# Optimization experiments

Measured on AMD Instinct MI355X. Metric: run time of the kernel, lower is better.

Reference implementation:

```python
import jax, jax.numpy as jnp
import numpy as np

N_NODES = 40000
N_EDGES = 400000
N_GRAPHS = 128
IN_F = 768
HID = 128
HEADS = 4
NEG_SLOPE = 0.2  # DGL GATConv default


def _p(key, shape, scale=0.02):
    return jax.random.normal(key, shape, dtype=jnp.float32) * scale


def setup_inputs() -> dict:
    key = jax.random.key(0)
    ks = jax.random.split(key, 20)
    x = jax.random.normal(ks[0], (N_NODES, IN_F), dtype=jnp.float32)
    src = jax.random.randint(ks[1], (N_EDGES,), 0, N_NODES)
    dst = jax.random.randint(ks[2], (N_EDGES,), 0, N_NODES)
    graph_ids = jnp.sort(jax.random.randint(ks[3], (N_NODES,), 0, N_GRAPHS))
    params = {
        # GAT layer 1: 768 -> 4 heads x 128
        "W1": _p(ks[4], (IN_F, HEADS * HID)),
        "al1": _p(ks[5], (HEADS, HID)),
        "ar1": _p(ks[6], (HEADS, HID)),
        "b1": jnp.zeros((HEADS * HID,), jnp.float32),
        # GAT layer 2: 512 -> 1 head x 128
        "W2": _p(ks[7], (HEADS * HID, HID)),
        "al2": _p(ks[8], (1, HID)),
        "ar2": _p(ks[9], (1, HID)),
        "b2": jnp.zeros((HID,), jnp.float32),
        # node MLP: 128 -> 128 -> 2
        "nW1": _p(ks[10], (HID, HID)), "nb1": jnp.zeros((HID,), jnp.float32),
        "nW2": _p(ks[11], (HID, 2)), "nb2": jnp.zeros((2,), jnp.float32),
        # graph MLP: 128 -> 128 -> 2
        "gW1": _p(ks[12], (HID, HID)), "gb1": jnp.zeros((HID,), jnp.float32),
        "gW2": _p(ks[13], (HID, 2)), "gb2": jnp.zeros((2,), jnp.float32),
    }
    return dict(x=x, src=src, dst=dst, graph_ids=graph_ids, **params)


def gat_conv(h, W, attn_l, attn_r, bias, src, dst, heads, out_f):
    # DGL GATConv (eval mode, no dropout): project, per-edge attention logits,
    # segment softmax over incoming edges of each dst node, weighted scatter-add.
    feat = (h @ W).reshape(N_NODES, heads, out_f)           # [N,H,F]
    el = jnp.einsum('nhf,hf->nh', feat, attn_l)              # [N,H]
    er = jnp.einsum('nhf,hf->nh', feat, attn_r)              # [N,H]
    e = el[src] + er[dst]                                    # [E,H]
    e = jnp.where(e > 0, e, NEG_SLOPE * e)                   # LeakyReLU(0.2)
    emax = jax.ops.segment_max(e, dst, num_segments=N_NODES)  # [N,H], -inf for empty
    ee = jnp.exp(e - emax[dst])                              # [E,H]
    denom = jax.ops.segment_sum(ee, dst, num_segments=N_NODES)  # [N,H]
    alpha = ee / denom[dst]                                  # [E,H]
    msg = feat[src] * alpha[:, :, None]                      # [E,H,F]
    out = jax.ops.segment_sum(msg, dst, num_segments=N_NODES)  # [N,H,F]
    return out + bias.reshape(1, heads, out_f)


def reference(x, src, dst, graph_ids, W1, al1, ar1, b1, W2, al2, ar2, b2,
              nW1, nb1, nW2, nb2, gW1, gb1, gW2, gb2):
    h = gat_conv(x, W1, al1, ar1, b1, src, dst, HEADS, HID)   # [N,4,128]
    h = h.reshape(N_NODES, HEADS * HID)                       # flatten(1)
    h = gat_conv(h, W2, al2, ar2, b2, src, dst, 1, HID)       # [N,1,128]
    h = h.squeeze(1)                                          # [N,128]
    # dgl.mean_nodes over batched graphs
    cnt = jax.ops.segment_sum(jnp.ones((N_NODES,), h.dtype), graph_ids, num_segments=N_GRAPHS)
    hg = jax.ops.segment_sum(h, graph_ids, num_segments=N_GRAPHS) / jnp.maximum(cnt, 1.0)[:, None]
    node_logits = jax.nn.relu(h @ nW1 + nb1) @ nW2 + nb2      # [N,2]
    graph_logits = jax.nn.relu(hg @ gW1 + gb1) @ gW2 + gb2    # [G,2]
    return node_logits, graph_logits
```

## Files before the change

kernel.cpp:

```cpp
#include <hip/hip_runtime.h>
#include <cstddef>

#define NN 40000
#define NE 400000
#define NG 128
#define NB_SCAN 157

typedef __attribute__((ext_vector_type(8))) short bf16x8;
typedef __attribute__((ext_vector_type(4))) float f32x4;

__device__ __forceinline__ void split1(float x, unsigned short& h, unsigned short& l)
{
    unsigned u = __float_as_uint(x);
    unsigned rh = u + 0x7FFFu + ((u >> 16) & 1u);
    h = (unsigned short)(rh >> 16);
    float fh = __uint_as_float(((unsigned)h) << 16);
    float r = x - fh;
    unsigned u2 = __float_as_uint(r);
    unsigned rl = u2 + 0x7FFFu + ((u2 >> 16) & 1u);
    l = (unsigned short)(rl >> 16);
}

__global__ void conv_bt(const float* __restrict__ B, unsigned short* __restrict__ hi,
                        unsigned short* __restrict__ lo, int K, int N)
{
    int e = blockIdx.x * 256 + threadIdx.x;
    if (e >= K * N) return;
    int n = e / K, k = e - n * K;
    unsigned short h, l;
    split1(B[(size_t)k * N + n], h, l);
    hi[e] = h; lo[e] = l;
}

#define LDK 40

__global__ __launch_bounds__(256) void gemm_split(
    const float* __restrict__ A, const unsigned short* __restrict__ Bh,
    const unsigned short* __restrict__ Bl, float* __restrict__ C,
    int M, int K, int N)
{
    __shared__ unsigned short Ah_s[128 * LDK];
    __shared__ unsigned short Al_s[128 * LDK];
    __shared__ unsigned short Bh_s[128 * LDK];
    __shared__ unsigned short Bl_s[128 * LDK];

    const int t    = threadIdx.x;
    const int lane = t & 63;
    const int wid  = t >> 6;
    const int wr   = wid >> 1, wc = wid & 1;
    const int bm   = blockIdx.x * 128, bn = blockIdx.y * 128;

    const int sr = t >> 1;
    const int sk = (t & 1) * 16;

    const int arow = bm + sr;
    const bool aval = (arow < M);
    const float* Ap = A + (size_t)arow * K + sk;
    const unsigned short* Bhp = Bh + (size_t)(bn + sr) * K + sk;
    const unsigned short* Blp = Bl + (size_t)(bn + sr) * K + sk;

    f32x4 acc[4][4];
    #pragma unroll
    for (int i = 0; i < 4; ++i)
        #pragma unroll
        for (int j = 0; j < 4; ++j) acc[i][j] = (f32x4){0.f, 0.f, 0.f, 0.f};

    float4 abuf[4];
    uint4 bhbuf[2], blbuf[2];
    const int NT = K / 32;

    auto load_tile = [&](int kt) {
        const int kb = kt * 32;
        if (aval) {
            #pragma unroll
            for (int q = 0; q < 4; ++q) abuf[q] = *(const float4*)(Ap + kb + q * 4);
        } else {
            #pragma unroll
            for (int q = 0; q < 4; ++q) abuf[q] = make_float4(0.f, 0.f, 0.f, 0.f);
        }
        bhbuf[0] = *(const uint4*)(Bhp + kb);
        bhbuf[1] = *(const uint4*)(Bhp + kb + 8);
        blbuf[0] = *(const uint4*)(Blp + kb);
        blbuf[1] = *(const uint4*)(Blp + kb + 8);
    };

    auto store_tile = [&]() {
        unsigned short h[16], l[16];
        #pragma unroll
        for (int q = 0; q < 4; ++q) {
            split1(abuf[q].x, h[q * 4 + 0], l[q * 4 + 0]);
            split1(abuf[q].y, h[q * 4 + 1], l[q * 4 + 1]);
            split1(abuf[q].z, h[q * 4 + 2], l[q * 4 + 2]);
            split1(abuf[q].w, h[q * 4 + 3], l[q * 4 + 3]);
        }
        *(uint4*)&Ah_s[sr * LDK + sk]     = *(uint4*)&h[0];
        *(uint4*)&Ah_s[sr * LDK + sk + 8] = *(uint4*)&h[8];
        *(uint4*)&Al_s[sr * LDK + sk]     = *(uint4*)&l[0];
        *(uint4*)&Al_s[sr * LDK + sk + 8] = *(uint4*)&l[8];
        *(uint4*)&Bh_s[sr * LDK + sk]     = bhbuf[0];
        *(uint4*)&Bh_s[sr * LDK + sk + 8] = bhbuf[1];
        *(uint4*)&Bl_s[sr * LDK + sk]     = blbuf[0];
        *(uint4*)&Bl_s[sr * LDK + sk + 8] = blbuf[1];
    };

    auto compute = [&]() {
        const int fr = lane & 15;
        const int fk = (lane >> 4) * 8;
        bf16x8 bhf[4], blf[4];
        #pragma unroll
        for (int ni = 0; ni < 4; ++ni) {
            bhf[ni] = *(bf16x8*)&Bh_s[(wc * 64 + ni * 16 + fr) * LDK + fk];
            blf[ni] = *(bf16x8*)&Bl_s[(wc * 64 + ni * 16 + fr) * LDK + fk];
        }
        #pragma unroll
        for (int mi = 0; mi < 4; ++mi) {
            bf16x8 ah = *(bf16x8*)&Ah_s[(wr * 64 + mi * 16 + fr) * LDK + fk];
            bf16x8 al = *(bf16x8*)&Al_s[(wr * 64 + mi * 16 + fr) * LDK + fk];
            #pragma unroll
            for (int ni = 0; ni < 4; ++ni) {
                acc[mi][ni] = __builtin_amdgcn_mfma_f32_16x16x32_bf16(ah, bhf[ni], acc[mi][ni], 0, 0, 0);
                acc[mi][ni] = __builtin_amdgcn_mfma_f32_16x16x32_bf16(ah, blf[ni], acc[mi][ni], 0, 0, 0);
                acc[mi][ni] = __builtin_amdgcn_mfma_f32_16x16x32_bf16(al, bhf[ni], acc[mi][ni], 0, 0, 0);
            }
        }
    };

    load_tile(0);
    store_tile();
    __syncthreads();
    for (int kt = 0;;) {
        if (kt + 1 < NT) load_tile(kt + 1);
        compute();
        ++kt;
        if (kt == NT) break;
        __syncthreads();
        store_tile();
        __syncthreads();
    }

    const int fr = lane & 15;
    const int fq = lane >> 4;
    #pragma unroll
    for (int mi = 0; mi < 4; ++mi) {
        int r0 = bm + wr * 64 + mi * 16 + fq * 4;
        #pragma unroll
        for (int ni = 0; ni < 4; ++ni) {
            int c = bn + wc * 64 + ni * 16 + fr;
            #pragma unroll
            for (int q = 0; q < 4; ++q) {
                int r = r0 + q;
                if (r < M) C[(size_t)r * N + c] = acc[mi][ni][q];
            }
        }
    }
}

__global__ void hist_kernel(const int* __restrict__ dst, int* __restrict__ cnt)
{
    int e = blockIdx.x * 256 + threadIdx.x;
    if (e < NE) atomicAdd(&cnt[dst[e]], 1);
}

__global__ __launch_bounds__(256) void scanA_kernel(
    const int* __restrict__ cnt, int* __restrict__ row, int* __restrict__ bsum)
{
    __shared__ int s[256];
    int t = threadIdx.x;
    int i = blockIdx.x * 256 + t;
    int v = (i < NN) ? cnt[i] : 0;
    s[t] = v;
    __syncthreads();
    #pragma unroll
    for (int off = 1; off < 256; off <<= 1) {
        int x = (t >= off) ? s[t - off] : 0;
        __syncthreads();
        s[t] += x;
        __syncthreads();
    }
    if (i < NN) row[i] = s[t] - v;
    if (t == 255) bsum[blockIdx.x] = s[255];
}

__global__ __launch_bounds__(256) void scanB_kernel(int* __restrict__ bsum)
{
    __shared__ int s[256];
    int t = threadIdx.x;
    int v = (t < NB_SCAN) ? bsum[t] : 0;
    s[t] = v;
    __syncthreads();
    #pragma unroll
    for (int off = 1; off < 256; off <<= 1) {
        int x = (t >= off) ? s[t - off] : 0;
        __syncthreads();
        s[t] += x;
        __syncthreads();
    }
    if (t < NB_SCAN) bsum[t] = s[t] - v;
}

__global__ void scanC_kernel(int* __restrict__ row, const int* __restrict__ bsum,
                             int* __restrict__ fill)
{
    int i = blockIdx.x * 256 + threadIdx.x;
    if (i < NN) {
        int r = row[i] + bsum[blockIdx.x];
        row[i] = r;
        fill[i] = r;
    }
    if (i == 0) row[NN] = NE;
}

__global__ void permute_kernel(const int* __restrict__ dst, int* __restrict__ fill,
                               int* __restrict__ eidx)
{
    int e = blockIdx.x * 256 + threadIdx.x;
    if (e < NE) {
        int pos = atomicAdd(&fill[dst[e]], 1);
        eidx[pos] = e;
    }
}

template <int H>
__global__ __launch_bounds__(256) void eler_kernel(
    const float* __restrict__ feat, const float* __restrict__ al,
    const float* __restrict__ ar, float* __restrict__ el, float* __restrict__ er)
{
    int wid  = (blockIdx.x * 256 + threadIdx.x) >> 6;
    int lane = threadIdx.x & 63;
    if (wid >= NN * H) return;
    int n = wid / H, h = wid % H;
    const float* f = feat + (size_t)n * (H * 128) + h * 128;
    float2 fv = *(const float2*)&f[lane * 2];
    float2 a1 = *(const float2*)&al[h * 128 + lane * 2];
    float2 a2 = *(const float2*)&ar[h * 128 + lane * 2];
    float sl = fv.x * a1.x + fv.y * a1.y;
    float sr = fv.x * a2.x + fv.y * a2.y;
    #pragma unroll
    for (int off = 32; off > 0; off >>= 1) {
        sl += __shfl_down(sl, off);
        sr += __shfl_down(sr, off);
    }
    if (lane == 0) { el[wid] = sl; er[wid] = sr; }
}

template <int H>
__global__ __launch_bounds__(256) void edge_w_kernel(
    const int* __restrict__ src, const int* __restrict__ dst,
    const float* __restrict__ el, const float* __restrict__ er,
    float* __restrict__ w)
{
    int e = blockIdx.x * 256 + threadIdx.x;
    if (e >= NE) return;
    int s = src[e], d = dst[e];
    if constexpr (H == 4) {
        float4 a = *(const float4*)&el[s * 4];
        float4 b = *(const float4*)&er[d * 4];
        float4 v = make_float4(a.x + b.x, a.y + b.y, a.z + b.z, a.w + b.w);
        v.x = v.x > 0.f ? v.x : 0.2f * v.x;
        v.y = v.y > 0.f ? v.y : 0.2f * v.y;
        v.z = v.z > 0.f ? v.z : 0.2f * v.z;
        v.w = v.w > 0.f ? v.w : 0.2f * v.w;
        *(float4*)&w[e * 4] = make_float4(__expf(v.x), __expf(v.y), __expf(v.z), __expf(v.w));
    } else {
        float v = el[s] + er[d];
        v = v > 0.f ? v : 0.2f * v;
        w[e] = __expf(v);
    }
}

template <int H>
__global__ __launch_bounds__(256) void agg_kernel(
    const int* __restrict__ row, const int* __restrict__ eidx,
    const int* __restrict__ src, const float* __restrict__ w,
    const float* __restrict__ feat, const float* __restrict__ bias,
    float* __restrict__ out)
{
    int wave = (blockIdx.x * 256 + threadIdx.x) >> 6;
    int lane = threadIdx.x & 63;
    if (wave >= NN) return;
    int r0 = row[wave], r1 = row[wave + 1];

    if constexpr (H == 4) {
        float d0 = 0.f, d1 = 0.f, d2 = 0.f, d3 = 0.f;
        for (int i = r0 + lane; i < r1; i += 64) {
            float4 wv = *(const float4*)&w[eidx[i] * 4];
            d0 += wv.x; d1 += wv.y; d2 += wv.z; d3 += wv.w;
        }
        #pragma unroll
        for (int off = 32; off > 0; off >>= 1) {
            d0 += __shfl_xor(d0, off);
            d1 += __shfl_xor(d1, off);
            d2 += __shfl_xor(d2, off);
            d3 += __shfl_xor(d3, off);
        }
        float4 a0 = {0.f,0.f,0.f,0.f}, a1 = {0.f,0.f,0.f,0.f};
        for (int i = r0; i < r1; ++i) {
            int e = eidx[i];
            int s = src[e];
            float4 wv = *(const float4*)&w[e * 4];
            const float* f = feat + (size_t)s * 512;
            float4 v0 = *(const float4*)&f[lane * 4];
            float4 v1 = *(const float4*)&f[256 + lane * 4];
            float alo = (lane & 32) ? wv.y : wv.x;
            float ahi = (lane & 32) ? wv.w : wv.z;
            a0.x = fmaf(v0.x, alo, a0.x); a0.y = fmaf(v0.y, alo, a0.y);
            a0.z = fmaf(v0.z, alo, a0.z); a0.w = fmaf(v0.w, alo, a0.w);
            a1.x = fmaf(v1.x, ahi, a1.x); a1.y = fmaf(v1.y, ahi, a1.y);
            a1.z = fmaf(v1.z, ahi, a1.z); a1.w = fmaf(v1.w, ahi, a1.w);
        }
        float ilo = (lane & 32) ? d1 : d0;
        float ihi = (lane & 32) ? d3 : d2;
        ilo = (r1 > r0) ? 1.0f / ilo : 0.0f;
        ihi = (r1 > r0) ? 1.0f / ihi : 0.0f;
        float4 b0 = *(const float4*)&bias[lane * 4];
        float4 b1v = *(const float4*)&bias[256 + lane * 4];
        float* o = out + (size_t)wave * 512;
        *(float4*)&o[lane * 4] = make_float4(
            fmaf(a0.x, ilo, b0.x), fmaf(a0.y, ilo, b0.y),
            fmaf(a0.z, ilo, b0.z), fmaf(a0.w, ilo, b0.w));
        *(float4*)&o[256 + lane * 4] = make_float4(
            fmaf(a1.x, ihi, b1v.x), fmaf(a1.y, ihi, b1v.y),
            fmaf(a1.z, ihi, b1v.z), fmaf(a1.w, ihi, b1v.w));
    } else {
        float den = 0.f;
        for (int i = r0 + lane; i < r1; i += 64) den += w[eidx[i]];
        #pragma unroll
        for (int off = 32; off > 0; off >>= 1) den += __shfl_xor(den, off);
        float2 a = {0.f, 0.f};
        for (int i = r0; i < r1; ++i) {
            int e = eidx[i];
            int s = src[e];
            float wv = w[e];
            float2 v = *(const float2*)&feat[(size_t)s * 128 + lane * 2];
            a.x = fmaf(v.x, wv, a.x);
            a.y = fmaf(v.y, wv, a.y);
        }
        float inv = (r1 > r0) ? 1.0f / den : 0.0f;
        float2 b = *(const float2*)&bias[lane * 2];
        float* o = out + (size_t)wave * 128;
        *(float2*)&o[lane * 2] = make_float2(fmaf(a.x, inv, b.x), fmaf(a.y, inv, b.y));
    }
}

__global__ __launch_bounds__(128) void graph_mean_kernel(
    const int* __restrict__ gid, const float* __restrict__ h2, float* __restrict__ hg)
{
    int g = blockIdx.x;
    int t = threadIdx.x;
    int lo = 0, hi = NN;
    while (lo < hi) { int m = (lo + hi) >> 1; if (gid[m] < g) lo = m + 1; else hi = m; }
    int start = lo;
    lo = start; hi = NN;
    while (lo < hi) { int m = (lo + hi) >> 1; if (gid[m] < g + 1) lo = m + 1; else hi = m; }
    int end = lo;
    float acc = 0.f;
    for (int n = start; n < end; ++n) acc += h2[(size_t)n * 128 + t];
    float c = fmaxf((float)(end - start), 1.0f);
    hg[g * 128 + t] = acc / c;
}

__global__ __launch_bounds__(128) void node_mlp_kernel(
    const float* __restrict__ h, const float* __restrict__ W1,
    const float* __restrict__ b1, const float* __restrict__ W2,
    const float* __restrict__ b2, float* __restrict__ out)
{
    __shared__ float row[128];
    __shared__ float hid[128];
    int n = blockIdx.x;
    int t = threadIdx.x;
    row[t] = h[(size_t)n * 128 + t];
    __syncthreads();
    float acc = b1[t];
    #pragma unroll 8
    for (int k = 0; k < 128; ++k) acc = fmaf(row[k], W1[k * 128 + t], acc);
    hid[t] = fmaxf(acc, 0.f);
    __syncthreads();
    if (t < 2) {
        float o = b2[t];
        for (int k = 0; k < 128; ++k) o = fmaf(hid[k], W2[k * 2 + t], o);
        out[(size_t)n * 2 + t] = o;
    }
}

__global__ __launch_bounds__(128) void graph_mlp_kernel(
    const float* __restrict__ hg,
    const float* __restrict__ W1, const float* __restrict__ b1,
    const float* __restrict__ W2, const float* __restrict__ b2,
    float* __restrict__ out)
{
    __shared__ float row[128];
    __shared__ float hid[128];
    int g = blockIdx.x;
    int t = threadIdx.x;
    row[t] = hg[(size_t)g * 128 + t];
    __syncthreads();
    float acc = b1[t];
    #pragma unroll 8
    for (int k = 0; k < 128; ++k) acc = fmaf(row[k], W1[k * 128 + t], acc);
    hid[t] = fmaxf(acc, 0.f);
    __syncthreads();
    if (t < 2) {
        float o = b2[t];
        for (int k = 0; k < 128; ++k) o = fmaf(hid[k], W2[k * 2 + t], o);
        out[(size_t)g * 2 + t] = o;
    }
}

static constexpr size_t O_FEAT1 = 0;
static constexpr size_t O_H1    = 20480000;
static constexpr size_t O_H2    = 5120000;
static constexpr size_t O_B2T   = 10240000;
static constexpr size_t O_EW    = 40960000;
static constexpr size_t O_HG    = 42880000;
static constexpr size_t O_INT   = 42896384;
static constexpr size_t I_ROW  = 0;
static constexpr size_t I_BSUM = 40064;
static constexpr size_t I_CNT  = 40224;
static constexpr size_t I_FILL = 80224;
static constexpr size_t I_EIDX = 120224;

extern "C" void kernel_launch(void* const* d_in, const int* in_sizes, int n_in,
                              void* d_out, int out_size, void* d_ws, size_t ws_size,
                              hipStream_t stream)
{
    const float* x    = (const float*)d_in[0];
    const int*   src  = (const int*)d_in[1];
    const int*   dst  = (const int*)d_in[2];
    const int*   gid  = (const int*)d_in[3];
    const float* W1   = (const float*)d_in[4];
    const float* al1  = (const float*)d_in[5];
    const float* ar1  = (const float*)d_in[6];
    const float* b1   = (const float*)d_in[7];
    const float* W2   = (const float*)d_in[8];
    const float* al2  = (const float*)d_in[9];
    const float* ar2  = (const float*)d_in[10];
    const float* b2   = (const float*)d_in[11];
    const float* nW1  = (const float*)d_in[12];
    const float* nb1  = (const float*)d_in[13];
    const float* nW2  = (const float*)d_in[14];
    const float* nb2  = (const float*)d_in[15];
    const float* gW1  = (const float*)d_in[16];
    const float* gb1  = (const float*)d_in[17];
    const float* gW2  = (const float*)d_in[18];
    const float* gb2  = (const float*)d_in[19];
    float* out = (float*)d_out;
    float* ws  = (float*)d_ws;

    float* feat1 = ws + O_FEAT1;
    float* h1    = ws + O_H1;
    float* feat2 = ws + O_FEAT1;
    float* h2    = ws + O_H2;
    float* el1   = ws + O_EW;
    float* er1   = ws + O_EW + 160000;
    float* w1e   = ws + O_EW + 320000;
    float* el2   = ws + O_EW;
    float* er2   = ws + O_EW + 40000;
    float* w2e   = ws + O_EW + 80000;
    float* hg    = ws + O_HG;
    int*   ibase = (int*)(ws + O_INT);
    int*   row   = ibase + I_ROW;
    int*   bsum  = ibase + I_BSUM;
    int*   cnt   = ibase + I_CNT;
    int*   fill  = ibase + I_FILL;
    int*   eidx  = ibase + I_EIDX;

    unsigned short* B1h = (unsigned short*)(ws + O_H1);
    unsigned short* B1l = B1h + 512 * 768;
    unsigned short* B2h = (unsigned short*)(ws + O_B2T);
    unsigned short* B2l = B2h + 128 * 512;

    hipMemsetAsync(cnt, 0, NN * sizeof(int), stream);
    hist_kernel<<<(NE + 255) / 256, 256, 0, stream>>>(dst, cnt);
    scanA_kernel<<<NB_SCAN, 256, 0, stream>>>(cnt, row, bsum);
    scanB_kernel<<<1, 256, 0, stream>>>(bsum);
    scanC_kernel<<<NB_SCAN, 256, 0, stream>>>(row, bsum, fill);
    permute_kernel<<<(NE + 255) / 256, 256, 0, stream>>>(dst, fill, eidx);

    conv_bt<<<(512 * 768 + 255) / 256, 256, 0, stream>>>(W1, B1h, B1l, 768, 512);
    gemm_split<<<dim3(313, 4), 256, 0, stream>>>(x, B1h, B1l, feat1, NN, 768, 512);
    eler_kernel<4><<<(NN * 4 * 64 + 255) / 256, 256, 0, stream>>>(feat1, al1, ar1, el1, er1);
    edge_w_kernel<4><<<(NE + 255) / 256, 256, 0, stream>>>(src, dst, el1, er1, w1e);
    agg_kernel<4><<<10000, 256, 0, stream>>>(row, eidx, src, w1e, feat1, b1, h1);

    conv_bt<<<(128 * 512 + 255) / 256, 256, 0, stream>>>(W2, B2h, B2l, 512, 128);
    gemm_split<<<dim3(313, 1), 256, 0, stream>>>(h1, B2h, B2l, feat2, NN, 512, 128);
    eler_kernel<1><<<(NN * 64 + 255) / 256, 256, 0, stream>>>(feat2, al2, ar2, el2, er2);
    edge_w_kernel<1><<<(NE + 255) / 256, 256, 0, stream>>>(src, dst, el2, er2, w2e);
    agg_kernel<1><<<10000, 256, 0, stream>>>(row, eidx, src, w2e, feat2, b2, h2);

    graph_mean_kernel<<<NG, 128, 0, stream>>>(gid, h2, hg);
    node_mlp_kernel<<<NN, 128, 0, stream>>>(h2, nW1, nb1, nW2, nb2, out);
    graph_mlp_kernel<<<NG, 128, 0, stream>>>(hg, gW1, gb1, gW2, gb2, out + (size_t)NN * 2);
}
```

Before: 0.9996 ms.

## Batch edge index loads per wave and swizzle GEMM blocks across XCDs

Result: faster. 940.8 us (-5.9%).

```diff
diff --git a/kernel.cpp b/kernel.cpp
--- a/kernel.cpp
+++ b/kernel.cpp
@@ -37,18 +37,30 @@
 __global__ __launch_bounds__(256) void gemm_split(
     const float* __restrict__ A, const unsigned short* __restrict__ Bh,
     const unsigned short* __restrict__ Bl, float* __restrict__ C,
-    int M, int K, int N)
+    int M, int K, int N, int swz)
 {
     __shared__ unsigned short Ah_s[128 * LDK];
     __shared__ unsigned short Al_s[128 * LDK];
     __shared__ unsigned short Bh_s[128 * LDK];
     __shared__ unsigned short Bl_s[128 * LDK];
 
+    int bm, bn;
+    if (swz) {
+        int xcd = blockIdx.x & 7;
+        int loc = blockIdx.x >> 3;
+        int bmi = xcd * 40 + (loc >> 2);
+        if (bmi >= 313) return;
+        bm = bmi * 128;
+        bn = (loc & 3) * 128;
+    } else {
+        bm = blockIdx.x * 128;
+        bn = blockIdx.y * 128;
+    }
+
     const int t    = threadIdx.x;
     const int lane = t & 63;
     const int wid  = t >> 6;
     const int wr   = wid >> 1, wc = wid & 1;
-    const int bm   = blockIdx.x * 128, bn = blockIdx.y * 128;
 
     const int sr = t >> 1;
     const int sk = (t & 1) * 16;
@@ -279,12 +291,58 @@
     int lane = threadIdx.x & 63;
     if (wave >= NN) return;
     int r0 = row[wave], r1 = row[wave + 1];
+    int nedge = r1 - r0;
 
     if constexpr (H == 4) {
         float d0 = 0.f, d1 = 0.f, d2 = 0.f, d3 = 0.f;
-        for (int i = r0 + lane; i < r1; i += 64) {
-            float4 wv = *(const float4*)&w[eidx[i] * 4];
+        float4 a0 = {0.f,0.f,0.f,0.f}, a1 = {0.f,0.f,0.f,0.f};
+        for (int base = 0; base < nedge; base += 64) {
+            int cnt = nedge - base; if (cnt > 64) cnt = 64;
+            int s = 0;
+            float4 wv = {0.f,0.f,0.f,0.f};
+            if (lane < cnt) {
+                int e = eidx[r0 + base + lane];
+                s = src[e];
+                wv = *(const float4*)&w[e * 4];
+            }
             d0 += wv.x; d1 += wv.y; d2 += wv.z; d3 += wv.w;
+            int j = 0;
+            for (; j + 1 < cnt; j += 2) {
+                int s0 = __shfl(s, j), s1 = __shfl(s, j + 1);
+                float wx0 = __shfl(wv.x, j), wy0 = __shfl(wv.y, j);
+                float wz0 = __shfl(wv.z, j), ww0 = __shfl(wv.w, j);
+                float wx1 = __shfl(wv.x, j + 1), wy1 = __shfl(wv.y, j + 1);
+                float wz1 = __shfl(wv.z, j + 1), ww1 = __shfl(wv.w, j + 1);
+                const float* f0 = feat + (size_t)s0 * 512;
+                const float* f1 = feat + (size_t)s1 * 512;
+                float4 p00 = *(const float4*)&f0[lane * 4];
+                float4 p01 = *(const float4*)&f0[256 + lane * 4];
+                float4 p10 = *(const float4*)&f1[lane * 4];
+                float4 p11 = *(const float4*)&f1[256 + lane * 4];
+                float alo0 = (lane & 32) ? wy0 : wx0, ahi0 = (lane & 32) ? ww0 : wz0;
+                float alo1 = (lane & 32) ? wy1 : wx1, ahi1 = (lane & 32) ? ww1 : wz1;
+                a0.x = fmaf(p00.x, alo0, a0.x); a0.y = fmaf(p00.y, alo0, a0.y);
+                a0.z = fmaf(p00.z, alo0, a0.z); a0.w = fmaf(p00.w, alo0, a0.w);
+                a1.x = fmaf(p01.x, ahi0, a1.x); a1.y = fmaf(p01.y, ahi0, a1.y);
+                a1.z = fmaf(p01.z, ahi0, a1.z); a1.w = fmaf(p01.w, ahi0, a1.w);
+                a0.x = fmaf(p10.x, alo1, a0.x); a0.y = fmaf(p10.y, alo1, a0.y);
+                a0.z = fmaf(p10.z, alo1, a0.z); a0.w = fmaf(p10.w, alo1, a0.w);
+                a1.x = fmaf(p11.x, ahi1, a1.x); a1.y = fmaf(p11.y, ahi1, a1.y);
+                a1.z = fmaf(p11.z, ahi1, a1.z); a1.w = fmaf(p11.w, ahi1, a1.w);
+            }
+            if (j < cnt) {
+                int s0 = __shfl(s, j);
+                float wx0 = __shfl(wv.x, j), wy0 = __shfl(wv.y, j);
+                float wz0 = __shfl(wv.z, j), ww0 = __shfl(wv.w, j);
+                const float* f0 = feat + (size_t)s0 * 512;
+                float4 p00 = *(const float4*)&f0[lane * 4];
+                float4 p01 = *(const float4*)&f0[256 + lane * 4];
+                float alo0 = (lane & 32) ? wy0 : wx0, ahi0 = (lane & 32) ? ww0 : wz0;
+                a0.x = fmaf(p00.x, alo0, a0.x); a0.y = fmaf(p00.y, alo0, a0.y);
+                a0.z = fmaf(p00.z, alo0, a0.z); a0.w = fmaf(p00.w, alo0, a0.w);
+                a1.x = fmaf(p01.x, ahi0, a1.x); a1.y = fmaf(p01.y, ahi0, a1.y);
+                a1.z = fmaf(p01.z, ahi0, a1.z); a1.w = fmaf(p01.w, ahi0, a1.w);
+            }
         }
         #pragma unroll
         for (int off = 32; off > 0; off >>= 1) {
@@ -293,25 +351,10 @@
             d2 += __shfl_xor(d2, off);
             d3 += __shfl_xor(d3, off);
         }
-        float4 a0 = {0.f,0.f,0.f,0.f}, a1 = {0.f,0.f,0.f,0.f};
-        for (int i = r0; i < r1; ++i) {
-            int e = eidx[i];
-            int s = src[e];
-            float4 wv = *(const float4*)&w[e * 4];
-            const float* f = feat + (size_t)s * 512;
-            float4 v0 = *(const float4*)&f[lane * 4];
-            float4 v1 = *(const float4*)&f[256 + lane * 4];
-            float alo = (lane & 32) ? wv.y : wv.x;
-            float ahi = (lane & 32) ? wv.w : wv.z;
-            a0.x = fmaf(v0.x, alo, a0.x); a0.y = fmaf(v0.y, alo, a0.y);
-            a0.z = fmaf(v0.z, alo, a0.z); a0.w = fmaf(v0.w, alo, a0.w);
-            a1.x = fmaf(v1.x, ahi, a1.x); a1.y = fmaf(v1.y, ahi, a1.y);
-            a1.z = fmaf(v1.z, ahi, a1.z); a1.w = fmaf(v1.w, ahi, a1.w);
-        }
         float ilo = (lane & 32) ? d1 : d0;
         float ihi = (lane & 32) ? d3 : d2;
-        ilo = (r1 > r0) ? 1.0f / ilo : 0.0f;
-        ihi = (r1 > r0) ? 1.0f / ihi : 0.0f;
+        ilo = (nedge > 0) ? 1.0f / ilo : 0.0f;
+        ihi = (nedge > 0) ? 1.0f / ihi : 0.0f;
         float4 b0 = *(const float4*)&bias[lane * 4];
         float4 b1v = *(const float4*)&bias[256 + lane * 4];
         float* o = out + (size_t)wave * 512;
@@ -323,19 +366,36 @@
             fmaf(a1.z, ihi, b1v.z), fmaf(a1.w, ihi, b1v.w));
     } else {
         float den = 0.f;
-        for (int i = r0 + lane; i < r1; i += 64) den += w[eidx[i]];
+        float2 a = {0.f, 0.f};
+        for (int base = 0; base < nedge; base += 64) {
+            int cnt = nedge - base; if (cnt > 64) cnt = 64;
+            int s = 0;
+            float wv = 0.f;
+            if (lane < cnt) {
+                int e = eidx[r0 + base + lane];
+                s = src[e];
+                wv = w[e];
+            }
+            den += wv;
+            int j = 0;
+            for (; j + 1 < cnt; j += 2) {
+                int s0 = __shfl(s, j), s1 = __shfl(s, j + 1);
+                float w0 = __shfl(wv, j), w1 = __shfl(wv, j + 1);
+                float2 p0 = *(const float2*)&feat[(size_t)s0 * 128 + lane * 2];
+                float2 p1 = *(const float2*)&feat[(size_t)s1 * 128 + lane * 2];
+                a.x = fmaf(p0.x, w0, a.x); a.y = fmaf(p0.y, w0, a.y);
+                a.x = fmaf(p1.x, w1, a.x); a.y = fmaf(p1.y, w1, a.y);
+            }
+            if (j < cnt) {
+                int s0 = __shfl(s, j);
+                float w0 = __shfl(wv, j);
+                float2 p0 = *(const float2*)&feat[(size_t)s0 * 128 + lane * 2];
+                a.x = fmaf(p0.x, w0, a.x); a.y = fmaf(p0.y, w0, a.y);
+            }
+        }
         #pragma unroll
         for (int off = 32; off > 0; off >>= 1) den += __shfl_xor(den, off);
-        float2 a = {0.f, 0.f};
-        for (int i = r0; i < r1; ++i) {
-            int e = eidx[i];
-            int s = src[e];
-            float wv = w[e];
-            float2 v = *(const float2*)&feat[(size_t)s * 128 + lane * 2];
-            a.x = fmaf(v.x, wv, a.x);
-            a.y = fmaf(v.y, wv, a.y);
-        }
-        float inv = (r1 > r0) ? 1.0f / den : 0.0f;
+        float inv = (nedge > 0) ? 1.0f / den : 0.0f;
         float2 b = *(const float2*)&bias[lane * 2];
         float* o = out + (size_t)wave * 128;
         *(float2*)&o[lane * 2] = make_float2(fmaf(a.x, inv, b.x), fmaf(a.y, inv, b.y));
@@ -477,13 +537,13 @@
     permute_kernel<<<(NE + 255) / 256, 256, 0, stream>>>(dst, fill, eidx);
 
     conv_bt<<<(512 * 768 + 255) / 256, 256, 0, stream>>>(W1, B1h, B1l, 768, 512);
-    gemm_split<<<dim3(313, 4), 256, 0, stream>>>(x, B1h, B1l, feat1, NN, 768, 512);
+    gemm_split<<<1280, 256, 0, stream>>>(x, B1h, B1l, feat1, NN, 768, 512, 1);
     eler_kernel<4><<<(NN * 4 * 64 + 255) / 256, 256, 0, stream>>>(feat1, al1, ar1, el1, er1);
     edge_w_kernel<4><<<(NE + 255) / 256, 256, 0, stream>>>(src, dst, el1, er1, w1e);
     agg_kernel<4><<<10000, 256, 0, stream>>>(row, eidx, src, w1e, feat1, b1, h1);
 
     conv_bt<<<(128 * 512 + 255) / 256, 256, 0, stream>>>(W2, B2h, B2l, 512, 128);
-    gemm_split<<<dim3(313, 1), 256, 0, stream>>>(h1, B2h, B2l, feat2, NN, 512, 128);
+    gemm_split<<<dim3(313, 1), 256, 0, stream>>>(h1, B2h, B2l, feat2, NN, 512, 128, 0);
     eler_kernel<1><<<(NN * 64 + 255) / 256, 256, 0, stream>>>(feat2, al2, ar2, el2, er2);
     edge_w_kernel<1><<<(NE + 255) / 256, 256, 0, stream>>>(src, dst, el2, er2, w2e);
     agg_kernel<1><<<10000, 256, 0, stream>>>(row, eidx, src, w2e, feat2, b2, h2);
```
